# Kernel tuning notes

Hardware: AMD Instinct MI355X
Metric: run time of the kernel (lower is better)

Reference implementation:

```python
import jax, jax.numpy as jnp
import numpy as np

ALPHA = 4.0  # spikingjelly surrogate.Sigmoid default
TAU = 2.0    # LIFNode default

@jax.custom_vjp
def spike(x):
    return (x >= 0).astype(x.dtype)

def _spike_fwd(x):
    return spike(x), x

def _spike_bwd(x, g):
    s = jax.nn.sigmoid(ALPHA * x)
    return (g * ALPHA * s * (1.0 - s),)

spike.defvjp(_spike_fwd, _spike_bwd)

def lif(x_seq, v_th):
    # multi-step LIF over leading time dim; decay_input=True, v_reset=0 (hard reset)
    def step(v, x):
        v = v + (x - v) / TAU
        s = spike(v - v_th)
        return v * (1.0 - s), s
    _, s_seq = jax.lax.scan(step, jnp.zeros_like(x_seq[0]), x_seq)
    return s_seq

def bn_c(x, gamma, beta, mean, var, eps=1e-5):
    # eval-mode BatchNorm1d over channel axis 2 of [T,N,C,V]
    inv = (gamma / jnp.sqrt(var + eps))[None, None, :, None]
    return (x - mean[None, None, :, None]) * inv + beta[None, None, :, None]

def conv1x1(x, w):
    # 1x1 Conv1d == channel mixing: w [Cout,Cin], x [T,N,C,V]
    return jnp.einsum('oc,tncv->tnov', w, x)

def setup_inputs() -> dict:
    key = jax.random.key(0)
    T, N, C, V = 4, 512, 256, 25
    ks = jax.random.split(key, 24)
    def bn_params(k1, k2, k3, k4):
        return (jax.random.uniform(k1, (C,)) * 0.5 + 0.75,
                jax.random.normal(k2, (C,)) * 0.1,
                jax.random.normal(k3, (C,)) * 0.1,
                jax.random.uniform(k4, (C,)) * 0.5 + 0.5)
    x = jax.random.normal(ks[0], (T, N, C, V), dtype=jnp.float32)
    s = 1.0 / np.sqrt(C)
    wq = jax.random.normal(ks[1], (C, C)) * s
    wk = jax.random.normal(ks[2], (C, C)) * s
    wv = jax.random.normal(ks[3], (C, C)) * s
    wp = jax.random.normal(ks[4], (C, C)) * s
    bp = jax.random.normal(ks[5], (C,)) * 0.02
    qg, qb, qm, qvar = bn_params(ks[6], ks[7], ks[8], ks[9])
    kg, kb, km, kvar = bn_params(ks[10], ks[11], ks[12], ks[13])
    vg, vb, vm, vvar = bn_params(ks[14], ks[15], ks[16], ks[17])
    pg, pb, pm, pvar = bn_params(ks[18], ks[19], ks[20], ks[21])
    return dict(x=x, wq=wq, wk=wk, wv=wv, wp=wp, bp=bp,
                qg=qg, qb=qb, qm=qm, qvar=qvar,
                kg=kg, kb=kb, km=km, kvar=kvar,
                vg=vg, vb=vb, vm=vm, vvar=vvar,
                pg=pg, pb=pb, pm=pm, pvar=pvar)

def reference(x, wq, wk, wv, wp, bp, qg, qb, qm, qvar, kg, kb, km, kvar,
              vg, vb, vm, vvar, pg, pb, pm, pvar):
    T, N, C, V = x.shape
    H = 8
    D = C // H
    scale = 0.125

    def branch(w, g, b, m, var):
        s = lif(bn_c(conv1x1(x, w), g, b, m, var), 1.0)       # [T,N,C,V]
        # -> [T,N,V,C] -> [T,N,V,H,D] -> [T,N,H,V,D]
        return jnp.transpose(s, (0, 1, 3, 2)).reshape(T, N, V, H, D).transpose(0, 1, 3, 2, 4)

    q = branch(wq, qg, qb, qm, qvar)
    k = branch(wk, kg, kb, km, kvar)
    v = branch(wv, vg, vb, vm, vvar)

    attn = jnp.einsum('tnhvd,tnhwd->tnhvw', q, k)            # binary spike attn, no softmax
    y = jnp.einsum('tnhvw,tnhwd->tnhvd', attn, v) * scale    # [T,N,H,V,D]
    y = y.transpose(0, 1, 2, 4, 3).reshape(T, N, C, V)       # transpose(3,4) then merge H*D=C
    y = lif(y, 0.5)                                          # attn_lif, v_threshold=0.5
    y = conv1x1(y, wp) + bp[None, None, :, None]             # proj_conv (bias=True)
    y = lif(bn_c(y, pg, pb, pm, pvar), 1.0)                  # proj_bn + proj_lif
    return y + x                                             # residual
```

## Files before the change

kernel.cpp:

```cpp
#include <hip/hip_runtime.h>
#include <cstdint>
#include <cstddef>

#define T_ 4
#define N_ 512
#define C_ 256
#define V_ 25
#define H_ 8

typedef _Float16 half8_t __attribute__((ext_vector_type(8)));
typedef float f32x16 __attribute__((ext_vector_type(16)));

__device__ __forceinline__ f32x16 mfma16(half8_t a, half8_t b, f32x16 c) {
  return __builtin_amdgcn_mfma_f32_32x32x16_f16(a, b, c, 0, 0, 0);
}

__global__ void kw_stage(const float* __restrict__ wq, const float* __restrict__ wk,
                         const float* __restrict__ wv, const float* __restrict__ wp,
                         const float* __restrict__ qg, const float* __restrict__ qvar,
                         const float* __restrict__ kg, const float* __restrict__ kvar,
                         const float* __restrict__ vg, const float* __restrict__ vvar,
                         const float* __restrict__ pg, const float* __restrict__ pvar,
                         _Float16* __restrict__ Wstg) {
  int i = blockIdx.x * 512 + threadIdx.x;
  int j = i & 7, lane = (i >> 3) & 63, rt = (i >> 9) & 3, m = (i >> 11) & 1;
  int s = (i >> 12) & 3, p = (i >> 14) & 3, c = i >> 16;
  int kt = p * 4 + s;
  int row = rt * 32 + (lane & 31);
  int k = kt * 16 + (lane >> 5) * 8 + j;
  const float *w, *g, *va;
  int grow;
  if (c < 6) {
    int br = c >> 1;
    w = br == 0 ? wq : br == 1 ? wk : wv;
    g = br == 0 ? qg : br == 1 ? kg : vg;
    va = br == 0 ? qvar : br == 1 ? kvar : vvar;
    grow = (c & 1) * 128 + row;
  } else {
    w = wp; g = pg; va = pvar;
    grow = (c - 6) * 128 + row;
  }
  float sc = g[grow] / sqrtf(va[grow] + 1e-5f);
  float wv_ = w[grow * 256 + k] * sc;
  _Float16 hi = (_Float16)wv_;
  Wstg[i] = (m == 0) ? hi : (_Float16)(wv_ - (float)hi);
}

__global__ void kx_stage(const float* __restrict__ x, _Float16* __restrict__ X16) {
  __shared__ float Xt[256 * 28];
  const int n = blockIdx.x, tid = threadIdx.x;
  for (int t = 0; t < 4; ++t) {
    __syncthreads();
    for (int i = tid; i < 6400; i += 256) {
      int k = i / 25, v = i - k * 25;
      Xt[k * 28 + v] = x[(size_t)(t * N_ + n) * 6400 + i];
    }
    __syncthreads();
    for (int jj = tid; jj < 800; jj += 256) {
      int kt = jj / 50, r = jj - kt * 50;
      int v = r >> 1, lkg = r & 1;
      int k0 = kt * 16 + lkg * 8;
      half8_t hi, lo;
#pragma unroll
      for (int e = 0; e < 8; ++e) {
        float f = Xt[(k0 + e) * 28 + v];
        _Float16 h = (_Float16)f;
        hi[e] = h;
        lo[e] = (_Float16)(f - (float)h);
      }
      int col = t * 25 + v;
      size_t bhi = ((((size_t)n * 2 + 0) * 16 + kt) * 100 + col) * 16 + lkg * 8;
      size_t blo = ((((size_t)n * 2 + 1) * 16 + kt) * 100 + col) * 16 + lkg * 8;
      *(half8_t*)(X16 + bhi) = hi;
      *(half8_t*)(X16 + blo) = lo;
    }
  }
}

#define STAGE_A(gidx, bufsel)                                                     \
  do {                                                                            \
    const _Float16* sp_ = Wstg + (size_t)(gidx) * 16384 + tid * 8;                \
    char* dp_ = Abuf + (bufsel) * 32768 + tid * 16;                               \
    __builtin_amdgcn_global_load_lds((const uint32_t*)(sp_),          (uint32_t*)(dp_),          16, 0, 0); \
    __builtin_amdgcn_global_load_lds((const uint32_t*)(sp_ + 4096),   (uint32_t*)(dp_ + 8192),   16, 0, 0); \
    __builtin_amdgcn_global_load_lds((const uint32_t*)(sp_ + 8192),   (uint32_t*)(dp_ + 16384),  16, 0, 0); \
    __builtin_amdgcn_global_load_lds((const uint32_t*)(sp_ + 12288),  (uint32_t*)(dp_ + 24576),  16, 0, 0); \
  } while (0)

#define MS_BYTE(colx, rowx) ((colx) * 256 + (((rowx) * 4) ^ (((colx) & 7) << 4)))

__launch_bounds__(512, 2)
__global__ void k1_mfma(const _Float16* __restrict__ X16, const _Float16* __restrict__ Wstg,
                        const float* __restrict__ qg, const float* __restrict__ qb,
                        const float* __restrict__ qm, const float* __restrict__ qvar,
                        const float* __restrict__ kg, const float* __restrict__ kb,
                        const float* __restrict__ km, const float* __restrict__ kvar,
                        const float* __restrict__ vg, const float* __restrict__ vb,
                        const float* __restrict__ vm, const float* __restrict__ vvar,
                        uint32_t* __restrict__ masks) {
  __shared__ __align__(16) char LDSb[65536 + 32768 + 512];
  char* Abuf = LDSb;
  char* MsB = LDSb + 65536;
  float* bic = (float*)(LDSb + 65536 + 32768);

  const int n = blockIdx.x, tid = threadIdx.x;
  const int lane = tid & 63, wid = tid >> 6;
  const int ks = wid & 1, cp = (wid >> 1) & 1, rt2 = wid >> 2;
  const int lr = lane & 31, lkg = lane >> 5;

  half8_t Bh[16], Bl[16];
#pragma unroll
  for (int ct = 0; ct < 2; ++ct) {
    int col = cp * 64 + ct * 32 + lr;
    if (col > 99) col = 99;
#pragma unroll
    for (int ktl = 0; ktl < 8; ++ktl) {
      int kt = ktl * 2 + ks;
      Bh[ct * 8 + ktl] = *(const half8_t*)(X16 + ((((size_t)n * 2 + 0) * 16 + kt) * 100 + col) * 16 + lkg * 8);
      Bl[ct * 8 + ktl] = *(const half8_t*)(X16 + ((((size_t)n * 2 + 1) * 16 + kt) * 100 + col) * 16 + lkg * 8);
    }
  }
  STAGE_A(0, 0);

  for (int c = 0; c < 6; ++c) {
    const int br = c >> 1;
    f32x16 acc00 = {}, acc01 = {}, acc10 = {}, acc11 = {};
#pragma unroll
    for (int p = 0; p < 4; ++p) {
      __syncthreads();
      if (p == 0 && tid < 128) {
        int ch = (c & 1) * 128 + tid;
        const float* g  = br == 0 ? qg : br == 1 ? kg : vg;
        const float* be = br == 0 ? qb : br == 1 ? kb : vb;
        const float* mu = br == 0 ? qm : br == 1 ? km : vm;
        const float* va = br == 0 ? qvar : br == 1 ? kvar : vvar;
        float sc = g[ch] / sqrtf(va[ch] + 1e-5f);
        bic[tid] = be[ch] - mu[ch] * sc;
      }
      int gnext = c * 4 + p + 1;
      if (gnext < 24) STAGE_A(gnext, (p + 1) & 1);
#pragma unroll
      for (int s2 = 0; s2 < 2; ++s2) {
        const int s = s2 * 2 + ks;
        const int bi = p * 2 + s2;
        const char* kb = Abuf + (p & 1) * 32768 + s * 8192 + (rt2 * 2) * 1024 + lane * 16;
        half8_t Ah0 = *(const half8_t*)(kb);
        half8_t Ah1 = *(const half8_t*)(kb + 1024);
        half8_t Al0 = *(const half8_t*)(kb + 4096);
        half8_t Al1 = *(const half8_t*)(kb + 4096 + 1024);
        __builtin_amdgcn_s_setprio(1);
        acc00 = mfma16(Ah0, Bh[bi], acc00);
        acc01 = mfma16(Ah0, Bh[8 + bi], acc01);
        acc10 = mfma16(Ah1, Bh[bi], acc10);
        acc11 = mfma16(Ah1, Bh[8 + bi], acc11);
        acc00 = mfma16(Ah0, Bl[bi], acc00);
        acc01 = mfma16(Ah0, Bl[8 + bi], acc01);
        acc10 = mfma16(Ah1, Bl[bi], acc10);
        acc11 = mfma16(Ah1, Bl[8 + bi], acc11);
        acc00 = mfma16(Al0, Bh[bi], acc00);
        acc01 = mfma16(Al0, Bh[8 + bi], acc01);
        acc10 = mfma16(Al1, Bh[bi], acc10);
        acc11 = mfma16(Al1, Bh[8 + bi], acc11);
        __builtin_amdgcn_s_setprio(0);
      }
    }

    __syncthreads();
    if (ks == 0) {
#pragma unroll
      for (int rsub = 0; rsub < 2; ++rsub) {
#pragma unroll
        for (int ct = 0; ct < 2; ++ct) {
          int col = cp * 64 + ct * 32 + lr;
          if (col < 100) {
            f32x16 A = rsub ? (ct ? acc11 : acc10) : (ct ? acc01 : acc00);
#pragma unroll
            for (int qq = 0; qq < 4; ++qq) {
              int rowb = (rt2 * 2 + rsub) * 32 + qq * 8 + lkg * 4;
              *(float4*)(MsB + MS_BYTE(col, rowb)) =
                  make_float4(A[qq * 4], A[qq * 4 + 1], A[qq * 4 + 2], A[qq * 4 + 3]);
            }
          }
        }
      }
    }
    __syncthreads();
    if (ks == 1) {
#pragma unroll
      for (int rsub = 0; rsub < 2; ++rsub) {
#pragma unroll
        for (int ct = 0; ct < 2; ++ct) {
          int col = cp * 64 + ct * 32 + lr;
          if (col < 100) {
            f32x16 A = rsub ? (ct ? acc11 : acc10) : (ct ? acc01 : acc00);
#pragma unroll
            for (int qq = 0; qq < 4; ++qq) {
              int rowb = (rt2 * 2 + rsub) * 32 + qq * 8 + lkg * 4;
              float4* mp = (float4*)(MsB + MS_BYTE(col, rowb));
              float4 old = *mp;
              *mp = make_float4(old.x + A[qq * 4], old.y + A[qq * 4 + 1],
                                old.z + A[qq * 4 + 2], old.w + A[qq * 4 + 3]);
            }
          }
        }
      }
    }
    __syncthreads();
    const int d = lane & 31, hl = lane >> 5;
    for (int it = 0; it < 7; ++it) {
      int task = it * 16 + wid * 2 + hl;
      bool valid = task < 100;
      int hg = valid ? task / 25 : 0;
      int v = valid ? task - hg * 25 : 0;
      int row = hg * 32 + d;
      float bicv = bic[row];
      float st = 0.0f;
#pragma unroll
      for (int t = 0; t < 4; ++t) {
        int colx = t * 25 + v;
        float cu = *(const float*)(MsB + MS_BYTE(colx, row)) + bicv;
        st += (cu - st) * 0.5f;
        bool sb = valid && (st >= 1.0f);
        if (st >= 1.0f) st = 0.0f;
        unsigned long long b = __ballot(sb);
        if (valid && (lane == 0 || lane == 32)) {
          uint32_t wd = (lane == 0) ? (uint32_t)b : (uint32_t)(b >> 32);
          masks[((((size_t)t * N_ + n) * 3 + br) * H_ + (c & 1) * 4 + hg) * V_ + v] = wd;
        }
      }
    }
  }
}

__launch_bounds__(64)
__global__ void k2_attn(const uint32_t* __restrict__ masks, uint32_t* __restrict__ mask2) {
  __shared__ uint32_t qs[T_][V_], ks_[T_][V_], vs[T_][V_];
  const int n = blockIdx.x >> 3;
  const int h = blockIdx.x & 7;
  const int l = threadIdx.x;
  for (int i = l; i < T_ * 3 * V_; i += 64) {
    int t = i / (3 * V_);
    int r = i - t * (3 * V_);
    int br = r / V_;
    int v = r - br * V_;
    uint32_t w = masks[(((size_t)t * N_ + n) * 3 + br) * (H_ * V_) + h * V_ + v];
    if (br == 0) qs[t][v] = w;
    else if (br == 1) ks_[t][v] = w;
    else vs[t][v] = w;
  }
  __syncthreads();
  const int hi = l >> 5, d = l & 31;
  for (int vv = 0; vv < 13; ++vv) {
    int v = vv * 2 + hi;
    bool valid = (v < V_);
    int vc = valid ? v : 0;
    float st = 0.0f;
#pragma unroll
    for (int t = 0; t < 4; ++t) {
      int y = 0;
      uint32_t qmw = qs[t][vc];
#pragma unroll
      for (int w = 0; w < V_; ++w) {
        int a = __popc(qmw & ks_[t][w]);
        y += a * (int)((vs[t][w] >> d) & 1u);
      }
      float yf = 0.125f * (float)y;
      st += (yf - st) * 0.5f;
      bool s = valid && (st >= 0.5f);
      if (st >= 0.5f) st = 0.0f;
      unsigned long long b = __ballot(s);
      if (valid && (l == 0 || l == 32)) {
        uint32_t wd = (l == 0) ? (uint32_t)b : (uint32_t)(b >> 32);
        mask2[(((size_t)t * N_ + n) * V_ + v) * H_ + h] = wd;
      }
    }
  }
}

__launch_bounds__(512, 2)
__global__ void k3_mfma(const float* __restrict__ x, const _Float16* __restrict__ Wstg,
                        const uint32_t* __restrict__ mask2, const float* __restrict__ bp,
                        const float* __restrict__ pg, const float* __restrict__ pb,
                        const float* __restrict__ pm, const float* __restrict__ pvar,
                        float* __restrict__ out) {
  __shared__ __align__(16) char LDSb[65536 + 32768 + 512 + 3200];
  char* Abuf = LDSb;
  char* MsB = LDSb + 65536;
  float* bic = (float*)(LDSb + 65536 + 32768);
  uint32_t* m2s = (uint32_t*)(LDSb + 65536 + 32768 + 512);

  const int n = blockIdx.x, tid = threadIdx.x;
  const int lane = tid & 63, wid = tid >> 6;
  const int rt = wid & 3, cp = wid >> 2;
  const int lr = lane & 31, lkg = lane >> 5;

  for (int i = tid; i < 800; i += 512) {
    int t = i / 200, r = i - t * 200;
    m2s[i] = mask2[(size_t)(t * N_ + n) * 200 + r];
  }
  __syncthreads();

  half8_t Bb[32];
#pragma unroll
  for (int ct = 0; ct < 2; ++ct) {
    int col = cp * 64 + ct * 32 + lr;
    bool valid = col < 100;
    int cc = valid ? col : 0;
    int t = cc / 25, v = cc - t * 25;
#pragma unroll
    for (int kt = 0; kt < 16; ++kt) {
#pragma unroll
      for (int jj = 0; jj < 8; ++jj) {
        int k = kt * 16 + lkg * 8 + jj;
        uint32_t bit = (m2s[t * 200 + v * 8 + (k >> 5)] >> (k & 31)) & 1u;
        Bb[ct * 16 + kt][jj] = (valid && bit) ? (_Float16)1.0f : (_Float16)0.0f;
      }
    }
  }
  STAGE_A(24, 0);

  for (int c = 0; c < 2; ++c) {
    f32x16 acc0 = {}, acc1 = {};
#pragma unroll
    for (int p = 0; p < 4; ++p) {
      __syncthreads();
      if (p == 0 && tid < 128) {
        int ch = c * 128 + tid;
        float sc = pg[ch] / sqrtf(pvar[ch] + 1e-5f);
        bic[tid] = fmaf(bp[ch] - pm[ch], sc, pb[ch]);
      }
      int gnext = (6 + c) * 4 + p + 1;
      if (gnext < 32) STAGE_A(gnext, (p + 1) & 1);
#pragma unroll
      for (int s = 0; s < 4; ++s) {
        const char* kb = Abuf + (p & 1) * 32768 + s * 8192 + rt * 1024 + lane * 16;
        half8_t Ahi = *(const half8_t*)(kb);
        half8_t Alo = *(const half8_t*)(kb + 4096);
        const int kt = p * 4 + s;
        __builtin_amdgcn_s_setprio(1);
        acc0 = mfma16(Ahi, Bb[kt], acc0);
        acc1 = mfma16(Ahi, Bb[16 + kt], acc1);
        acc0 = mfma16(Alo, Bb[kt], acc0);
        acc1 = mfma16(Alo, Bb[16 + kt], acc1);
        __builtin_amdgcn_s_setprio(0);
      }
    }

    __syncthreads();
#pragma unroll
    for (int ct = 0; ct < 2; ++ct) {
      int col = cp * 64 + ct * 32 + lr;
      if (col < 100) {
        f32x16 A = ct ? acc1 : acc0;
#pragma unroll
        for (int qq = 0; qq < 4; ++qq) {
          int rowb = rt * 32 + qq * 8 + lkg * 4;
          *(float4*)(MsB + MS_BYTE(col, rowb)) =
              make_float4(A[qq * 4], A[qq * 4 + 1], A[qq * 4 + 2], A[qq * 4 + 3]);
        }
      }
    }
    __syncthreads();
    const int d = lane & 31, hl = lane >> 5;
    for (int it = 0; it < 7; ++it) {
      int task = it * 16 + wid * 2 + hl;
      bool valid = task < 100;
      int hg = valid ? task / 25 : 0;
      int v = valid ? task - hg * 25 : 0;
      int row = hg * 32 + d;
      float bicv = bic[row];
      float st = 0.0f;
#pragma unroll
      for (int t = 0; t < 4; ++t) {
        int colx = t * 25 + v;
        char* mp = MsB + MS_BYTE(colx, row);
        if (valid) {
          float cu = *(const float*)(mp) + bicv;
          st += (cu - st) * 0.5f;
          float sv = (st >= 1.0f) ? 1.0f : 0.0f;
          if (st >= 1.0f) st = 0.0f;
          *(float*)(mp) = sv;
        }
      }
    }
    __syncthreads();
    for (int ii = tid; ii < 12800; ii += 512) {
      int t = ii / 3200, r2 = ii - t * 3200;
      int cl = r2 / 25, v = r2 - cl * 25;
      int colx = t * 25 + v;
      float sv = *(const float*)(MsB + MS_BYTE(colx, cl));
      size_t go = (size_t)(t * N_ + n) * 6400 + (size_t)(c * 128 + cl) * 25 + v;
      out[go] = sv + x[go];
    }
  }
}

extern "C" void kernel_launch(void* const* d_in, const int* in_sizes, int n_in,
                              void* d_out, int out_size, void* d_ws, size_t ws_size,
                              hipStream_t stream) {
  const float* x    = (const float*)d_in[0];
  const float* wq   = (const float*)d_in[1];
  const float* wk   = (const float*)d_in[2];
  const float* wv   = (const float*)d_in[3];
  const float* wp   = (const float*)d_in[4];
  const float* bp   = (const float*)d_in[5];
  const float* qg   = (const float*)d_in[6];
  const float* qb   = (const float*)d_in[7];
  const float* qm   = (const float*)d_in[8];
  const float* qvar = (const float*)d_in[9];
  const float* kg   = (const float*)d_in[10];
  const float* kb   = (const float*)d_in[11];
  const float* km   = (const float*)d_in[12];
  const float* kvar = (const float*)d_in[13];
  const float* vg   = (const float*)d_in[14];
  const float* vb   = (const float*)d_in[15];
  const float* vm   = (const float*)d_in[16];
  const float* vvar = (const float*)d_in[17];
  const float* pg   = (const float*)d_in[18];
  const float* pb   = (const float*)d_in[19];
  const float* pm   = (const float*)d_in[20];
  const float* pvar = (const float*)d_in[21];

  _Float16* Wstg = (_Float16*)d_ws;
  _Float16* X16  = (_Float16*)d_ws + 524288;
  uint32_t* masks = (uint32_t*)((char*)d_ws + 1048576 + 52428800);
  uint32_t* mask2 = masks + 1228800;

  kw_stage<<<1024, 512, 0, stream>>>(wq, wk, wv, wp, qg, qvar, kg, kvar,
                                     vg, vvar, pg, pvar, Wstg);
  kx_stage<<<512, 256, 0, stream>>>(x, X16);
  k1_mfma<<<512, 512, 0, stream>>>(X16, Wstg, qg, qb, qm, qvar, kg, kb, km, kvar,
                                   vg, vb, vm, vvar, masks);
  k2_attn<<<4096, 64, 0, stream>>>(masks, mask2);
  k3_mfma<<<512, 512, 0, stream>>>(x, Wstg, mask2, bp, pg, pb, pm, pvar, (float*)d_out);
}
```

Measured before the change: 294.3 us.

## Split GEMM kernels into smaller blocks and register-block the attention loop

Both MFMA GEMM kernels are reworked into 256-thread blocks that each handle half or a quarter of the output channels per sample. This doubles or quadruples the grid and uses much smaller LDS tiles, so more blocks fit per CU, with waves_per_eu fixed at 3. k1 now streams the fp16 low part of X from global memory on each phase instead of holding it in registers, and buffers its spike masks in LDS so they can be written out as a compact block. The attention kernel is restructured to keep 13 query rows in registers and reuse each key/value word across them. The cost is more redundant X loads and setup work across blocks, plus a changed mask layout that k1 and k2 must agree on.

```diff
diff --git a/kernel.cpp b/kernel.cpp
--- a/kernel.cpp
+++ b/kernel.cpp
@@ -77,106 +77,112 @@
   }
 }
 
-#define STAGE_A(gidx, bufsel)                                                     \
-  do {                                                                            \
-    const _Float16* sp_ = Wstg + (size_t)(gidx) * 16384 + tid * 8;                \
-    char* dp_ = Abuf + (bufsel) * 32768 + tid * 16;                               \
-    __builtin_amdgcn_global_load_lds((const uint32_t*)(sp_),          (uint32_t*)(dp_),          16, 0, 0); \
-    __builtin_amdgcn_global_load_lds((const uint32_t*)(sp_ + 4096),   (uint32_t*)(dp_ + 8192),   16, 0, 0); \
-    __builtin_amdgcn_global_load_lds((const uint32_t*)(sp_ + 8192),   (uint32_t*)(dp_ + 16384),  16, 0, 0); \
-    __builtin_amdgcn_global_load_lds((const uint32_t*)(sp_ + 12288),  (uint32_t*)(dp_ + 24576),  16, 0, 0); \
+#define MS_BYTE(colx, rowx) ((colx) * 256 + (((rowx) * 4) ^ (((colx) & 7) << 4)))
+
+#define STAGE_HALF(cc, kt0, bs)                                                     \
+  do {                                                                              \
+    int sb_ = tid >> 6;                                                             \
+    _Pragma("unroll")                                                               \
+    for (int q_ = 0; q_ < 2; ++q_) {                                                \
+      int kt_ = (kt0) + q_;                                                         \
+      const _Float16* sp_ = Wstg +                                                  \
+          ((size_t)(((((cc) * 4 + (kt_ >> 2)) * 4 + (kt_ & 3)) * 2 + (sb_ >> 1)) * 4 \
+                    + (rh * 2 + (sb_ & 1))) << 9) + ((tid & 63) << 3);              \
+      char* dp_ = Abuf + (bs) * 8192 + ((q_ * 4 + sb_) << 10) + ((tid & 63) << 4);  \
+      __builtin_amdgcn_global_load_lds((const uint32_t*)sp_, (uint32_t*)dp_, 16, 0, 0); \
+    }                                                                               \
   } while (0)
 
-#define MS_BYTE(colx, rowx) ((colx) * 256 + (((rowx) * 4) ^ (((colx) & 7) << 4)))
-
-__launch_bounds__(512, 2)
-__global__ void k1_mfma(const _Float16* __restrict__ X16, const _Float16* __restrict__ Wstg,
-                        const float* __restrict__ qg, const float* __restrict__ qb,
-                        const float* __restrict__ qm, const float* __restrict__ qvar,
-                        const float* __restrict__ kg, const float* __restrict__ kb,
-                        const float* __restrict__ km, const float* __restrict__ kvar,
-                        const float* __restrict__ vg, const float* __restrict__ vb,
-                        const float* __restrict__ vm, const float* __restrict__ vvar,
-                        uint32_t* __restrict__ masks) {
-  __shared__ __align__(16) char LDSb[65536 + 32768 + 512];
+__attribute__((amdgpu_waves_per_eu(3, 3)))
+__global__ __launch_bounds__(256) void k1q(
+    const _Float16* __restrict__ X16, const _Float16* __restrict__ Wstg,
+    const float* __restrict__ qg, const float* __restrict__ qb,
+    const float* __restrict__ qm, const float* __restrict__ qvar,
+    const float* __restrict__ kg, const float* __restrict__ kb,
+    const float* __restrict__ km, const float* __restrict__ kvar,
+    const float* __restrict__ vg, const float* __restrict__ vb,
+    const float* __restrict__ vm, const float* __restrict__ vvar,
+    uint32_t* __restrict__ masks) {
+  __shared__ __align__(16) char LDSb[16384 + 25600 + 1536 + 4800];
   char* Abuf = LDSb;
-  char* MsB = LDSb + 65536;
-  float* bic = (float*)(LDSb + 65536 + 32768);
-
-  const int n = blockIdx.x, tid = threadIdx.x;
+  char* MsB = LDSb + 16384;
+  float* bicL = (float*)(LDSb + 41984);
+  uint32_t* mkL = (uint32_t*)(LDSb + 43520);
+
+  const int n = blockIdx.x >> 1, rh = blockIdx.x & 1;
+  const int tid = threadIdx.x;
   const int lane = tid & 63, wid = tid >> 6;
-  const int ks = wid & 1, cp = (wid >> 1) & 1, rt2 = wid >> 2;
+  const int ks = wid & 1, cp = wid >> 1;
   const int lr = lane & 31, lkg = lane >> 5;
 
-  half8_t Bh[16], Bl[16];
-#pragma unroll
-  for (int ct = 0; ct < 2; ++ct) {
-    int col = cp * 64 + ct * 32 + lr;
-    if (col > 99) col = 99;
-#pragma unroll
-    for (int ktl = 0; ktl < 8; ++ktl) {
-      int kt = ktl * 2 + ks;
-      Bh[ct * 8 + ktl] = *(const half8_t*)(X16 + ((((size_t)n * 2 + 0) * 16 + kt) * 100 + col) * 16 + lkg * 8);
-      Bl[ct * 8 + ktl] = *(const half8_t*)(X16 + ((((size_t)n * 2 + 1) * 16 + kt) * 100 + col) * 16 + lkg * 8);
-    }
-  }
-  STAGE_A(0, 0);
+  for (int i = tid; i < 384; i += 256) {
+    int cc = i >> 6, rl = i & 63;
+    int br = cc >> 1, ch = (cc & 1) * 128 + rh * 64 + rl;
+    const float* g  = br == 0 ? qg : br == 1 ? kg : vg;
+    const float* be = br == 0 ? qb : br == 1 ? kb : vb;
+    const float* mu = br == 0 ? qm : br == 1 ? km : vm;
+    const float* va = br == 0 ? qvar : br == 1 ? kvar : vvar;
+    float sc = g[ch] / sqrtf(va[ch] + 1e-5f);
+    bicL[i] = be[ch] - mu[ch] * sc;
+  }
+
+  const _Float16* xhi = X16 + (size_t)(n * 2) * 25600;
+  const _Float16* xlo = xhi + 25600;
+  int col0 = cp * 64 + lr;       if (col0 > 99) col0 = 99;
+  int col1 = cp * 64 + 32 + lr;  if (col1 > 99) col1 = 99;
+  half8_t Bh[16];
+#pragma unroll
+  for (int ph = 0; ph < 8; ++ph) {
+    int kt = ph * 2 + ks;
+    Bh[ph]     = *(const half8_t*)(xhi + (kt * 100 + col0) * 16 + lkg * 8);
+    Bh[8 + ph] = *(const half8_t*)(xhi + (kt * 100 + col1) * 16 + lkg * 8);
+  }
+  STAGE_HALF(0, 0, 0);
 
   for (int c = 0; c < 6; ++c) {
     const int br = c >> 1;
     f32x16 acc00 = {}, acc01 = {}, acc10 = {}, acc11 = {};
 #pragma unroll
-    for (int p = 0; p < 4; ++p) {
+    for (int ph = 0; ph < 8; ++ph) {
       __syncthreads();
-      if (p == 0 && tid < 128) {
-        int ch = (c & 1) * 128 + tid;
-        const float* g  = br == 0 ? qg : br == 1 ? kg : vg;
-        const float* be = br == 0 ? qb : br == 1 ? kb : vb;
-        const float* mu = br == 0 ? qm : br == 1 ? km : vm;
-        const float* va = br == 0 ? qvar : br == 1 ? kvar : vvar;
-        float sc = g[ch] / sqrtf(va[ch] + 1e-5f);
-        bic[tid] = be[ch] - mu[ch] * sc;
-      }
-      int gnext = c * 4 + p + 1;
-      if (gnext < 24) STAGE_A(gnext, (p + 1) & 1);
-#pragma unroll
-      for (int s2 = 0; s2 < 2; ++s2) {
-        const int s = s2 * 2 + ks;
-        const int bi = p * 2 + s2;
-        const char* kb = Abuf + (p & 1) * 32768 + s * 8192 + (rt2 * 2) * 1024 + lane * 16;
-        half8_t Ah0 = *(const half8_t*)(kb);
-        half8_t Ah1 = *(const half8_t*)(kb + 1024);
-        half8_t Al0 = *(const half8_t*)(kb + 4096);
-        half8_t Al1 = *(const half8_t*)(kb + 4096 + 1024);
-        __builtin_amdgcn_s_setprio(1);
-        acc00 = mfma16(Ah0, Bh[bi], acc00);
-        acc01 = mfma16(Ah0, Bh[8 + bi], acc01);
-        acc10 = mfma16(Ah1, Bh[bi], acc10);
-        acc11 = mfma16(Ah1, Bh[8 + bi], acc11);
-        acc00 = mfma16(Ah0, Bl[bi], acc00);
-        acc01 = mfma16(Ah0, Bl[8 + bi], acc01);
-        acc10 = mfma16(Ah1, Bl[bi], acc10);
-        acc11 = mfma16(Ah1, Bl[8 + bi], acc11);
-        acc00 = mfma16(Al0, Bh[bi], acc00);
-        acc01 = mfma16(Al0, Bh[8 + bi], acc01);
-        acc10 = mfma16(Al1, Bh[bi], acc10);
-        acc11 = mfma16(Al1, Bh[8 + bi], acc11);
-        __builtin_amdgcn_s_setprio(0);
-      }
+      if (ph < 7) STAGE_HALF(c, (ph + 1) * 2, (ph + 1) & 1);
+      else if (c < 5) STAGE_HALF(c + 1, 0, 0);
+      const char* base = Abuf + (ph & 1) * 8192 + (ks << 12) + lane * 16;
+      half8_t Ah0 = *(const half8_t*)(base);
+      half8_t Ah1 = *(const half8_t*)(base + 1024);
+      half8_t Al0 = *(const half8_t*)(base + 2048);
+      half8_t Al1 = *(const half8_t*)(base + 3072);
+      int kt = ph * 2 + ks;
+      half8_t Bl0 = *(const half8_t*)(xlo + (kt * 100 + col0) * 16 + lkg * 8);
+      half8_t Bl1 = *(const half8_t*)(xlo + (kt * 100 + col1) * 16 + lkg * 8);
+      __builtin_amdgcn_s_setprio(1);
+      acc00 = mfma16(Ah0, Bh[ph], acc00);
+      acc01 = mfma16(Ah0, Bh[8 + ph], acc01);
+      acc10 = mfma16(Ah1, Bh[ph], acc10);
+      acc11 = mfma16(Ah1, Bh[8 + ph], acc11);
+      acc00 = mfma16(Ah0, Bl0, acc00);
+      acc01 = mfma16(Ah0, Bl1, acc01);
+      acc10 = mfma16(Ah1, Bl0, acc10);
+      acc11 = mfma16(Ah1, Bl1, acc11);
+      acc00 = mfma16(Al0, Bh[ph], acc00);
+      acc01 = mfma16(Al0, Bh[8 + ph], acc01);
+      acc10 = mfma16(Al1, Bh[ph], acc10);
+      acc11 = mfma16(Al1, Bh[8 + ph], acc11);
+      __builtin_amdgcn_s_setprio(0);
     }
 
     __syncthreads();
     if (ks == 0) {
 #pragma unroll
-      for (int rsub = 0; rsub < 2; ++rsub) {
+      for (int rtl = 0; rtl < 2; ++rtl) {
 #pragma unroll
         for (int ct = 0; ct < 2; ++ct) {
           int col = cp * 64 + ct * 32 + lr;
           if (col < 100) {
-            f32x16 A = rsub ? (ct ? acc11 : acc10) : (ct ? acc01 : acc00);
+            f32x16 A = rtl ? (ct ? acc11 : acc10) : (ct ? acc01 : acc00);
 #pragma unroll
             for (int qq = 0; qq < 4; ++qq) {
-              int rowb = (rt2 * 2 + rsub) * 32 + qq * 8 + lkg * 4;
+              int rowb = rtl * 32 + qq * 8 + lkg * 4;
               *(float4*)(MsB + MS_BYTE(col, rowb)) =
                   make_float4(A[qq * 4], A[qq * 4 + 1], A[qq * 4 + 2], A[qq * 4 + 3]);
             }
@@ -187,15 +193,15 @@
     __syncthreads();
     if (ks == 1) {
 #pragma unroll
-      for (int rsub = 0; rsub < 2; ++rsub) {
+      for (int rtl = 0; rtl < 2; ++rtl) {
 #pragma unroll
         for (int ct = 0; ct < 2; ++ct) {
           int col = cp * 64 + ct * 32 + lr;
           if (col < 100) {
-            f32x16 A = rsub ? (ct ? acc11 : acc10) : (ct ? acc01 : acc00);
+            f32x16 A = rtl ? (ct ? acc11 : acc10) : (ct ? acc01 : acc00);
 #pragma unroll
             for (int qq = 0; qq < 4; ++qq) {
-              int rowb = (rt2 * 2 + rsub) * 32 + qq * 8 + lkg * 4;
+              int rowb = rtl * 32 + qq * 8 + lkg * 4;
               float4* mp = (float4*)(MsB + MS_BYTE(col, rowb));
               float4 old = *mp;
               *mp = make_float4(old.x + A[qq * 4], old.y + A[qq * 4 + 1],
@@ -208,12 +214,12 @@
     __syncthreads();
     const int d = lane & 31, hl = lane >> 5;
     for (int it = 0; it < 7; ++it) {
-      int task = it * 16 + wid * 2 + hl;
-      bool valid = task < 100;
-      int hg = valid ? task / 25 : 0;
-      int v = valid ? task - hg * 25 : 0;
-      int row = hg * 32 + d;
-      float bicv = bic[row];
+      int task = it * 8 + wid * 2 + hl;
+      bool valid = task < 50;
+      int hgl = valid ? task / 25 : 0;
+      int v = valid ? task - hgl * 25 : 0;
+      int row = hgl * 32 + d;
+      float bicv = bicL[c * 64 + row];
       float st = 0.0f;
 #pragma unroll
       for (int t = 0; t < 4; ++t) {
@@ -225,10 +231,20 @@
         unsigned long long b = __ballot(sb);
         if (valid && (lane == 0 || lane == 32)) {
           uint32_t wd = (lane == 0) ? (uint32_t)b : (uint32_t)(b >> 32);
-          masks[((((size_t)t * N_ + n) * 3 + br) * H_ + (c & 1) * 4 + hg) * V_ + v] = wd;
+          mkL[t * 300 + br * 100 + (c & 1) * 50 + hgl * 25 + v] = wd;
         }
       }
     }
+  }
+
+  __syncthreads();
+  for (int i = tid; i < 1200; i += 256) {
+    int t = i / 300, r = i - t * 300;
+    int br = r / 100, r2 = r - br * 100;
+    int ch2 = r2 / 50, r3 = r2 - ch2 * 50;
+    int hgl = r3 / 25, v = r3 - hgl * 25;
+    masks[(size_t)(t * N_ + n) * 600 + br * 200 + ch2 * 100 + (rh * 2 + hgl) * 25 + v] =
+        mkL[i];
   }
 }
 
@@ -243,31 +259,40 @@
     int r = i - t * (3 * V_);
     int br = r / V_;
     int v = r - br * V_;
-    uint32_t w = masks[(((size_t)t * N_ + n) * 3 + br) * (H_ * V_) + h * V_ + v];
+    uint32_t w = masks[(size_t)(t * N_ + n) * 600 + br * 200 + h * V_ + v];
     if (br == 0) qs[t][v] = w;
     else if (br == 1) ks_[t][v] = w;
     else vs[t][v] = w;
   }
   __syncthreads();
   const int hi = l >> 5, d = l & 31;
-  for (int vv = 0; vv < 13; ++vv) {
-    int v = vv * 2 + hi;
-    bool valid = (v < V_);
-    int vc = valid ? v : 0;
-    float st = 0.0f;
-#pragma unroll
-    for (int t = 0; t < 4; ++t) {
-      int y = 0;
-      uint32_t qmw = qs[t][vc];
-#pragma unroll
-      for (int w = 0; w < V_; ++w) {
-        int a = __popc(qmw & ks_[t][w]);
-        y += a * (int)((vs[t][w] >> d) & 1u);
-      }
-      float yf = 0.125f * (float)y;
-      st += (yf - st) * 0.5f;
-      bool s = valid && (st >= 0.5f);
-      if (st >= 0.5f) st = 0.0f;
+  float st[13];
+#pragma unroll
+  for (int vv = 0; vv < 13; ++vv) st[vv] = 0.0f;
+#pragma unroll
+  for (int t = 0; t < 4; ++t) {
+    uint32_t q[13];
+    int y[13];
+#pragma unroll
+    for (int vv = 0; vv < 13; ++vv) {
+      int v = vv * 2 + hi;
+      q[vv] = qs[t][v < V_ ? v : 0];
+      y[vv] = 0;
+    }
+    for (int w = 0; w < V_; ++w) {
+      uint32_t kw = ks_[t][w];
+      int vb = (int)((vs[t][w] >> d) & 1u);
+#pragma unroll
+      for (int vv = 0; vv < 13; ++vv) y[vv] += __popc(q[vv] & kw) * vb;
+    }
+#pragma unroll
+    for (int vv = 0; vv < 13; ++vv) {
+      int v = vv * 2 + hi;
+      bool valid = (v < V_);
+      float yf = 0.125f * (float)y[vv];
+      st[vv] += (yf - st[vv]) * 0.5f;
+      bool s = valid && (st[vv] >= 0.5f);
+      if (st[vv] >= 0.5f) st[vv] = 0.0f;
       unsigned long long b = __ballot(s);
       if (valid && (l == 0 || l == 32)) {
         uint32_t wd = (l == 0) ? (uint32_t)b : (uint32_t)(b >> 32);
@@ -277,98 +302,97 @@
   }
 }
 
-__launch_bounds__(512, 2)
-__global__ void k3_mfma(const float* __restrict__ x, const _Float16* __restrict__ Wstg,
-                        const uint32_t* __restrict__ mask2, const float* __restrict__ bp,
-                        const float* __restrict__ pg, const float* __restrict__ pb,
-                        const float* __restrict__ pm, const float* __restrict__ pvar,
-                        float* __restrict__ out) {
-  __shared__ __align__(16) char LDSb[65536 + 32768 + 512 + 3200];
+__attribute__((amdgpu_waves_per_eu(3, 3)))
+__global__ __launch_bounds__(256) void k3q(
+    const float* __restrict__ x, const _Float16* __restrict__ Wstg,
+    const uint32_t* __restrict__ mask2, const float* __restrict__ bp,
+    const float* __restrict__ pg, const float* __restrict__ pb,
+    const float* __restrict__ pm, const float* __restrict__ pvar,
+    float* __restrict__ out) {
+  __shared__ __align__(16) char LDSb[16384 + 25600 + 256 + 3200];
   char* Abuf = LDSb;
-  char* MsB = LDSb + 65536;
-  float* bic = (float*)(LDSb + 65536 + 32768);
-  uint32_t* m2s = (uint32_t*)(LDSb + 65536 + 32768 + 512);
-
-  const int n = blockIdx.x, tid = threadIdx.x;
+  char* MsB = LDSb + 16384;
+  float* bicL = (float*)(LDSb + 41984);
+  uint32_t* m2s = (uint32_t*)(LDSb + 42240);
+
+  const int n = blockIdx.x >> 2, qv = blockIdx.x & 3;
+  const int c3 = qv >> 1, rh = qv & 1;
+  const int tid = threadIdx.x;
   const int lane = tid & 63, wid = tid >> 6;
-  const int rt = wid & 3, cp = wid >> 2;
   const int lr = lane & 31, lkg = lane >> 5;
 
-  for (int i = tid; i < 800; i += 512) {
+  for (int i = tid; i < 800; i += 256) {
     int t = i / 200, r = i - t * 200;
     m2s[i] = mask2[(size_t)(t * N_ + n) * 200 + r];
   }
-  __syncthreads();
-
-  half8_t Bb[32];
-#pragma unroll
-  for (int ct = 0; ct < 2; ++ct) {
-    int col = cp * 64 + ct * 32 + lr;
-    bool valid = col < 100;
-    int cc = valid ? col : 0;
-    int t = cc / 25, v = cc - t * 25;
-#pragma unroll
-    for (int kt = 0; kt < 16; ++kt) {
-#pragma unroll
-      for (int jj = 0; jj < 8; ++jj) {
-        int k = kt * 16 + lkg * 8 + jj;
-        uint32_t bit = (m2s[t * 200 + v * 8 + (k >> 5)] >> (k & 31)) & 1u;
-        Bb[ct * 16 + kt][jj] = (valid && bit) ? (_Float16)1.0f : (_Float16)0.0f;
-      }
-    }
-  }
-  STAGE_A(24, 0);
-
-  for (int c = 0; c < 2; ++c) {
-    f32x16 acc0 = {}, acc1 = {};
-#pragma unroll
-    for (int p = 0; p < 4; ++p) {
-      __syncthreads();
-      if (p == 0 && tid < 128) {
-        int ch = c * 128 + tid;
-        float sc = pg[ch] / sqrtf(pvar[ch] + 1e-5f);
-        bic[tid] = fmaf(bp[ch] - pm[ch], sc, pb[ch]);
-      }
-      int gnext = (6 + c) * 4 + p + 1;
-      if (gnext < 32) STAGE_A(gnext, (p + 1) & 1);
-#pragma unroll
-      for (int s = 0; s < 4; ++s) {
-        const char* kb = Abuf + (p & 1) * 32768 + s * 8192 + rt * 1024 + lane * 16;
-        half8_t Ahi = *(const half8_t*)(kb);
-        half8_t Alo = *(const half8_t*)(kb + 4096);
-        const int kt = p * 4 + s;
-        __builtin_amdgcn_s_setprio(1);
-        acc0 = mfma16(Ahi, Bb[kt], acc0);
-        acc1 = mfma16(Ahi, Bb[16 + kt], acc1);
-        acc0 = mfma16(Alo, Bb[kt], acc0);
-        acc1 = mfma16(Alo, Bb[16 + kt], acc1);
-        __builtin_amdgcn_s_setprio(0);
-      }
-    }
-
-    __syncthreads();
-#pragma unroll
-    for (int ct = 0; ct < 2; ++ct) {
-      int col = cp * 64 + ct * 32 + lr;
-      if (col < 100) {
-        f32x16 A = ct ? acc1 : acc0;
-#pragma unroll
-        for (int qq = 0; qq < 4; ++qq) {
-          int rowb = rt * 32 + qq * 8 + lkg * 4;
-          *(float4*)(MsB + MS_BYTE(col, rowb)) =
-              make_float4(A[qq * 4], A[qq * 4 + 1], A[qq * 4 + 2], A[qq * 4 + 3]);
-        }
-      }
-    }
-    __syncthreads();
+  if (tid < 64) {
+    int ch = qv * 64 + tid;
+    float sc = pg[ch] / sqrtf(pvar[ch] + 1e-5f);
+    bicL[tid] = fmaf(bp[ch] - pm[ch], sc, pb[ch]);
+  }
+  __syncthreads();
+
+  int col = wid * 32 + lr;
+  bool cvalid = col < 100;
+  int cc = cvalid ? col : 0;
+  int tq = cc / 25, vq = cc - tq * 25;
+  half8_t Bb[16];
+#pragma unroll
+  for (int kt = 0; kt < 16; ++kt) {
+#pragma unroll
+    for (int jj = 0; jj < 8; ++jj) {
+      int k = kt * 16 + lkg * 8 + jj;
+      uint32_t bit = (m2s[tq * 200 + vq * 8 + (k >> 5)] >> (k & 31)) & 1u;
+      Bb[kt][jj] = (cvalid && bit) ? (_Float16)1.0f : (_Float16)0.0f;
+    }
+  }
+  STAGE_HALF(6 + c3, 0, 0);
+
+  f32x16 acc0 = {}, acc1 = {};
+#pragma unroll
+  for (int ph = 0; ph < 8; ++ph) {
+    __syncthreads();
+    if (ph < 7) STAGE_HALF(6 + c3, (ph + 1) * 2, (ph + 1) & 1);
+#pragma unroll
+    for (int q2 = 0; q2 < 2; ++q2) {
+      const char* base = Abuf + (ph & 1) * 8192 + (q2 << 12) + lane * 16;
+      half8_t Ah0 = *(const half8_t*)(base);
+      half8_t Ah1 = *(const half8_t*)(base + 1024);
+      half8_t Al0 = *(const half8_t*)(base + 2048);
+      half8_t Al1 = *(const half8_t*)(base + 3072);
+      const int kt = ph * 2 + q2;
+      __builtin_amdgcn_s_setprio(1);
+      acc0 = mfma16(Ah0, Bb[kt], acc0);
+      acc1 = mfma16(Ah1, Bb[kt], acc1);
+      acc0 = mfma16(Al0, Bb[kt], acc0);
+      acc1 = mfma16(Al1, Bb[kt], acc1);
+      __builtin_amdgcn_s_setprio(0);
+    }
+  }
+
+  __syncthreads();
+  if (cvalid) {
+#pragma unroll
+    for (int rtl = 0; rtl < 2; ++rtl) {
+      f32x16 A = rtl ? acc1 : acc0;
+#pragma unroll
+      for (int qq = 0; qq < 4; ++qq) {
+        int rowb = rtl * 32 + qq * 8 + lkg * 4;
+        *(float4*)(MsB + MS_BYTE(col, rowb)) =
+            make_float4(A[qq * 4], A[qq * 4 + 1], A[qq * 4 + 2], A[qq * 4 + 3]);
+      }
+    }
+  }
+  __syncthreads();
+  {
     const int d = lane & 31, hl = lane >> 5;
     for (int it = 0; it < 7; ++it) {
-      int task = it * 16 + wid * 2 + hl;
-      bool valid = task < 100;
-      int hg = valid ? task / 25 : 0;
-      int v = valid ? task - hg * 25 : 0;
-      int row = hg * 32 + d;
-      float bicv = bic[row];
+      int task = it * 8 + wid * 2 + hl;
+      bool valid = task < 50;
+      int hgl = valid ? task / 25 : 0;
+      int v = valid ? task - hgl * 25 : 0;
+      int row = hgl * 32 + d;
+      float bicv = bicL[row];
       float st = 0.0f;
 #pragma unroll
       for (int t = 0; t < 4; ++t) {
@@ -383,15 +407,15 @@
         }
       }
     }
-    __syncthreads();
-    for (int ii = tid; ii < 12800; ii += 512) {
-      int t = ii / 3200, r2 = ii - t * 3200;
-      int cl = r2 / 25, v = r2 - cl * 25;
-      int colx = t * 25 + v;
-      float sv = *(const float*)(MsB + MS_BYTE(colx, cl));
-      size_t go = (size_t)(t * N_ + n) * 6400 + (size_t)(c * 128 + cl) * 25 + v;
-      out[go] = sv + x[go];
-    }
+  }
+  __syncthreads();
+  for (int ii = tid; ii < 6400; ii += 256) {
+    int t = ii / 1600, r2 = ii - t * 1600;
+    int cl = r2 / 25, v = r2 - cl * 25;
+    int colx = t * 25 + v;
+    float sv = *(const float*)(MsB + MS_BYTE(colx, cl));
+    size_t go = (size_t)(t * N_ + n) * 6400 + (size_t)(qv * 64 + cl) * 25 + v;
+    out[go] = sv + x[go];
   }
 }
 
@@ -429,8 +453,8 @@
   kw_stage<<<1024, 512, 0, stream>>>(wq, wk, wv, wp, qg, qvar, kg, kvar,
                                      vg, vvar, pg, pvar, Wstg);
   kx_stage<<<512, 256, 0, stream>>>(x, X16);
-  k1_mfma<<<512, 512, 0, stream>>>(X16, Wstg, qg, qb, qm, qvar, kg, kb, km, kvar,
-                                   vg, vb, vm, vvar, masks);
+  k1q<<<1024, 256, 0, stream>>>(X16, Wstg, qg, qb, qm, qvar, kg, kb, km, kvar,
+                                vg, vb, vm, vvar, masks);
   k2_attn<<<4096, 64, 0, stream>>>(masks, mask2);
-  k3_mfma<<<512, 512, 0, stream>>>(x, Wstg, mask2, bp, pg, pb, pm, pvar, (float*)d_out);
-}
+  k3q<<<2048, 256, 0, stream>>>(x, Wstg, mask2, bp, pg, pb, pm, pvar, (float*)d_out);
+}
```

Result: slower. 543.9 us (+84.8%).
